# Kernel tuning notes

Hardware: AMD Instinct MI355X
Metric: run time of the kernel (lower is better)

Reference implementation:

```python
import jax, jax.numpy as jnp
import numpy as np

B, S, D, H = 2, 2048, 1024, 16
DK = D // H


def setup_inputs() -> dict:
    key = jax.random.key(0)
    ks = jax.random.split(key, 12)
    sd = 1.0 / np.sqrt(D)
    inp = {
        "query": jax.random.normal(ks[0], (B, S, D), jnp.float32),
        "key": jax.random.normal(ks[1], (B, S, D), jnp.float32),
        "value": jax.random.normal(ks[2], (B, S, D), jnp.float32),
        # causal mask, broadcast over batch and heads: [1, 1, S, S]
        "mask": jnp.tril(jnp.ones((S, S), jnp.bool_))[None, None],
        "wq_w": jax.random.uniform(ks[3], (D, D), jnp.float32, -sd, sd),
        "wq_b": jax.random.uniform(ks[4], (D,), jnp.float32, -sd, sd),
        "wk_w": jax.random.uniform(ks[5], (D, D), jnp.float32, -sd, sd),
        "wk_b": jax.random.uniform(ks[6], (D,), jnp.float32, -sd, sd),
        "wv_w": jax.random.uniform(ks[7], (D, D), jnp.float32, -sd, sd),
        "wv_b": jax.random.uniform(ks[8], (D,), jnp.float32, -sd, sd),
        "wo_w": jax.random.uniform(ks[9], (D, D), jnp.float32, -sd, sd),
        "wo_b": jax.random.uniform(ks[10], (D,), jnp.float32, -sd, sd),
    }
    return inp


def reference(query, key, value, mask, wq_w, wq_b, wk_w, wk_b, wv_w, wv_b, wo_w, wo_b):
    # linear projections (torch Linear: x @ W^T + b), split into heads -> [B, H, S, DK]
    def proj(x, w, b):
        y = jnp.einsum("bsd,ed->bse", x, w) + b
        return y.reshape(B, S, H, DK).transpose(0, 2, 1, 3)

    q = proj(query, wq_w, wq_b)
    k = proj(key, wk_w, wk_b)
    v = proj(value, wv_w, wv_b)

    scale = 1.0 / np.sqrt(DK)
    scores = jnp.einsum("bhqd,bhkd->bhqk", q, k) * scale  # [B, H, S, S]
    scores = jnp.where(mask, scores, -jnp.inf)
    attn = jax.nn.softmax(scores, axis=-1)
    out = jnp.einsum("bhqk,bhkd->bhqd", attn, v)  # [B, H, S, DK]
    out = out.transpose(0, 2, 1, 3).reshape(B, S, D)
    # output projection; dropout is identity at eval / p=0
    return jnp.einsum("bsd,ed->bse", out, wo_w) + wo_b
```

## Files before the change

kernel.cpp:

```cpp
#include <hip/hip_runtime.h>


typedef unsigned short u16;
typedef unsigned int u32;
typedef __bf16 bf16x8 __attribute__((ext_vector_type(8)));
typedef float f32x4 __attribute__((ext_vector_type(4)));
typedef float f32x16 __attribute__((ext_vector_type(16)));
typedef float f32x2 __attribute__((ext_vector_type(2)));
typedef float f32x4v __attribute__((ext_vector_type(4)));
typedef u16 u16x4 __attribute__((ext_vector_type(4)));
typedef u32 u32x4 __attribute__((ext_vector_type(4)));
typedef int i32x4 __attribute__((ext_vector_type(4)));

#define B_ 2
#define S_ 2048
#define D_ 1024
#define H_ 16
#define DK_ 64

__device__ __forceinline__ u16 f2bf(float f) {
  __bf16 h = (__bf16)f;
  return __builtin_bit_cast(u16, h);
}

__device__ __forceinline__ float fexp2(float x) { return __builtin_amdgcn_exp2f(x); }

__device__ __forceinline__ f32x4 mfma16(bf16x8 a, bf16x8 b, f32x4 c) {
  return __builtin_amdgcn_mfma_f32_16x16x32_bf16(a, b, c, 0, 0, 0);
}
__device__ __forceinline__ f32x16 mfma32(bf16x8 a, bf16x8 b, f32x16 c) {
  return __builtin_amdgcn_mfma_f32_32x32x16_bf16(a, b, c, 0, 0, 0);
}

__device__ __forceinline__ u32 cvtpk(float lo, float hi) {
  u32 r;
  asm volatile("v_cvt_pk_bf16_f32 %0, %1, %2" : "=v"(r) : "v"(lo), "v"(hi));
  return r;
}
__device__ __forceinline__ u32 sx32(u32 v) { return (u32)__shfl_xor((int)v, 32, 64); }

typedef __attribute__((address_space(1))) void GV;
typedef __attribute__((address_space(3))) void LV;
__device__ __forceinline__ void gload16(const u16* g, u16* l) {
  __builtin_amdgcn_global_load_lds((GV*)g, (LV*)l, 16, 0, 0);
}

__global__ __launch_bounds__(256) void cast_all(const float* __restrict__ s0, const float* __restrict__ s1,
                                                const float* __restrict__ s2, const float* __restrict__ s3,
                                                const float* __restrict__ s4, const float* __restrict__ s5,
                                                const float* __restrict__ s6, u16* __restrict__ dst) {
  const int N0 = 1048576, N1 = 2097152, N2 = 3145728, N3 = 3407872, N4 = 3670016, N5 = 3932160, N6 = 4194304;
  int stride = gridDim.x * blockDim.x;
  for (int i = blockIdx.x * blockDim.x + threadIdx.x; i < N6; i += stride) {
    const float* src;
    int off;
    if (i < N0)      { src = s0; off = i; }
    else if (i < N1) { src = s1; off = i - N0; }
    else if (i < N2) { src = s2; off = i - N1; }
    else if (i < N3) { src = s3; off = i - N2; }
    else if (i < N4) { src = s4; off = i - N3; }
    else if (i < N5) { src = s5; off = i - N4; }
    else             { src = s6; off = i - N5; }
    f32x4v v = reinterpret_cast<const f32x4v*>(src)[off];
    u16x4 o;
    o.x = f2bf(v.x); o.y = f2bf(v.y); o.z = f2bf(v.z); o.w = f2bf(v.w);
    reinterpret_cast<u16x4*>(dst)[i] = o;
  }
}

__device__ __forceinline__ void gemm_tile_128(const u16* __restrict__ A,
                                              const u16* __restrict__ Bw,
                                              int K, int bm, int bn,
                                              f32x4 (&acc)[4][4],
                                              u16* ldsA, u16* ldsB) {
  const int tid = threadIdx.x;
  const int lane = tid & 63;
  const int w = tid >> 6;
  const int wm = w >> 1, wn = w & 1;
  const int fr = lane & 15, fq = lane >> 4;

  const u16* aBase = A + (size_t)(bm * 128) * K;
  const u16* bBase = Bw + (size_t)(bn * 128) * K;

  const int r0 = tid >> 2;
  const int cq0 = tid & 3;
  const int cs0 = (cq0 ^ (r0 & 3)) * 8;
  const int cs1 = (cq0 ^ ((r0 + 64) & 3)) * 8;

#define STAGE_G(buf, kk)                                                                          \
  do {                                                                                            \
    gload16(aBase + (size_t)r0 * K + (kk) + cs0, ldsA + (buf) * 4096 + tid * 8);                  \
    gload16(aBase + (size_t)(r0 + 64) * K + (kk) + cs1, ldsA + (buf) * 4096 + (tid + 256) * 8);   \
    gload16(bBase + (size_t)r0 * K + (kk) + cs0, ldsB + (buf) * 4096 + tid * 8);                  \
    gload16(bBase + (size_t)(r0 + 64) * K + (kk) + cs1, ldsB + (buf) * 4096 + (tid + 256) * 8);   \
  } while (0)

  STAGE_G(0, 0);
  STAGE_G(1, 32);

  const int nk = K >> 5;
  for (int t = 0; t < nk; ++t) {
    if (t + 1 < nk) { asm volatile("s_waitcnt vmcnt(4)" ::: "memory"); }
    else            { asm volatile("s_waitcnt vmcnt(0)" ::: "memory"); }
    __builtin_amdgcn_s_barrier();
    __builtin_amdgcn_sched_barrier(0);
    if (t + 2 < nk) {
      const int nb = (t + 2) % 3;
      STAGE_G(nb, (t + 2) * 32);
    }
    const u16* la = ldsA + (t % 3) * 4096;
    const u16* lb = ldsB + (t % 3) * 4096;
    bf16x8 af[4], bfv[4];
#pragma unroll
    for (int m = 0; m < 4; ++m) {
      int row = wm * 64 + m * 16 + fr;
      int cq = fq ^ (row & 3);
      af[m] = *reinterpret_cast<const bf16x8*>(la + (row * 4 + cq) * 8);
    }
#pragma unroll
    for (int n = 0; n < 4; ++n) {
      int row = wn * 64 + n * 16 + fr;
      int cq = fq ^ (row & 3);
      bfv[n] = *reinterpret_cast<const bf16x8*>(lb + (row * 4 + cq) * 8);
    }
    __builtin_amdgcn_s_setprio(1);
#pragma unroll
    for (int m = 0; m < 4; ++m)
#pragma unroll
      for (int n = 0; n < 4; ++n)
        acc[m][n] = mfma16(af[m], bfv[n], acc[m][n]);
    __builtin_amdgcn_s_setprio(0);
  }
#undef STAGE_G
}

__global__ __launch_bounds__(256) void gemm_qkv(const u16* __restrict__ Xq, const u16* __restrict__ Xk,
                                                const u16* __restrict__ Xv, const u16* __restrict__ Wq,
                                                const u16* __restrict__ Wk, const u16* __restrict__ Wv,
                                                const float* __restrict__ bq, const float* __restrict__ bk,
                                                const float* __restrict__ bv,
                                                u16* __restrict__ Qw, u16* __restrict__ Kw,
                                                u16* __restrict__ Vt) {
  __shared__ __align__(16) u16 ldsA[3 * 128 * 32];
  __shared__ __align__(16) u16 ldsB[3 * 128 * 32];
  const int z = blockIdx.z;
  const u16* A = (z == 0) ? Xq : (z == 1) ? Xk : Xv;
  const u16* W = (z == 0) ? Wq : (z == 1) ? Wk : Wv;
  const float* bias = (z == 0) ? bq : (z == 1) ? bk : bv;
  const float osc = (z == 0) ? (0.125f * 1.44269504f) : 1.0f;

  f32x4 acc[4][4];
#pragma unroll
  for (int m = 0; m < 4; ++m)
#pragma unroll
    for (int n = 0; n < 4; ++n)
      acc[m][n] = (f32x4){0.f, 0.f, 0.f, 0.f};

  gemm_tile_128(A, W, 1024, blockIdx.y, blockIdx.x, acc, ldsA, ldsB);

  const int lane = threadIdx.x & 63;
  const int w = threadIdx.x >> 6, wm = w >> 1, wn = w & 1;
  const int fr = lane & 15, fq = lane >> 4;
#pragma unroll
  for (int m = 0; m < 4; ++m) {
#pragma unroll
    for (int n = 0; n < 4; ++n) {
      int col = blockIdx.x * 128 + wn * 64 + n * 16 + fr;
      float bcol = bias[col];
      int h = col >> 6, dk = col & 63;
#pragma unroll
      for (int j = 0; j < 4; ++j) {
        int row = blockIdx.y * 128 + wm * 64 + m * 16 + fq * 4 + j;
        float v = (acc[m][n][j] + bcol) * osc;
        u16 bb = f2bf(v);
        int b = row >> 11, s = row & (S_ - 1);
        if (z == 0)      Qw[((b * H_ + h) * S_ + s) * DK_ + dk] = bb;
        else if (z == 1) Kw[((b * H_ + h) * S_ + s) * DK_ + dk] = bb;
        else             Vt[((b * H_ + h) * DK_ + dk) * S_ + s] = bb;
      }
    }
  }
}

__global__ __launch_bounds__(256) void gemm_out(const u16* __restrict__ O, const u16* __restrict__ Wo,
                                                const float* __restrict__ bo, float* __restrict__ Y) {
  __shared__ __align__(16) u16 ldsA[3 * 128 * 32];
  __shared__ __align__(16) u16 ldsB[3 * 128 * 32];
  f32x4 acc[4][4];
#pragma unroll
  for (int m = 0; m < 4; ++m)
#pragma unroll
    for (int n = 0; n < 4; ++n)
      acc[m][n] = (f32x4){0.f, 0.f, 0.f, 0.f};

  gemm_tile_128(O, Wo, 1024, blockIdx.y, blockIdx.x, acc, ldsA, ldsB);

  const int lane = threadIdx.x & 63;
  const int w = threadIdx.x >> 6, wm = w >> 1, wn = w & 1;
  const int fr = lane & 15, fq = lane >> 4;
#pragma unroll
  for (int m = 0; m < 4; ++m) {
#pragma unroll
    for (int n = 0; n < 4; ++n) {
      int col = blockIdx.x * 128 + wn * 64 + n * 16 + fr;
      float bcol = bo[col];
#pragma unroll
      for (int j = 0; j < 4; ++j) {
        int row = blockIdx.y * 128 + wm * 64 + m * 16 + fq * 4 + j;
        Y[(size_t)row * D_ + col] = acc[m][n][j] + bcol;
      }
    }
  }
}

__global__ __launch_bounds__(256) void attn_kernel(const u16* __restrict__ Qw,
                                                   const u16* __restrict__ Kw,
                                                   const u16* __restrict__ Vt,
                                                   u16* __restrict__ O) {
  __shared__ float mbuf[2][64][64];
  __shared__ float mlbuf[2][64];

  const int id = blockIdx.x;
  const int bh = (id & 7) * 4 + ((id >> 3) & 3);
  const int qb = 31 - (id >> 5);
  const int tid = threadIdx.x;
  const int w = tid >> 6;
  const int lane = tid & 63;
  const int col = lane & 31;
  const int hi = lane >> 5;

  const u16* Qg = Qw + ((size_t)bh * S_ + qb * 64) * DK_;
  const u16* Kg = Kw + (size_t)bh * S_ * DK_;
  const u16* Vg = Vt + (size_t)bh * DK_ * S_;
  const int b = bh >> 4, h = bh & 15;

  bf16x8 qf[2][4];
#pragma unroll
  for (int qt = 0; qt < 2; ++qt)
#pragma unroll
    for (int c = 0; c < 4; ++c)
      qf[qt][c] = *reinterpret_cast<const bf16x8*>(Qg + (qt * 32 + col) * DK_ + c * 16 + hi * 8);

  f32x16 o[2][2];
  float ll[2] = {0.f, 0.f};
#pragma unroll
  for (int qt = 0; qt < 2; ++qt)
#pragma unroll
    for (int dt = 0; dt < 2; ++dt)
#pragma unroll
      for (int r = 0; r < 16; ++r) o[qt][dt][r] = 0.f;

  for (int t = w; t <= qb; t += 4) {
    const u16* Kt = Kg + (size_t)t * 64 * DK_;
    const u16* Vtt = Vg + t * 64;
    bf16x8 pa[2][4];
#pragma unroll
    for (int kt = 0; kt < 2; ++kt) {
      bf16x8 ka[4];
#pragma unroll
      for (int c = 0; c < 4; ++c)
        ka[c] = *reinterpret_cast<const bf16x8*>(Kt + (kt * 32 + col) * DK_ + c * 16 + hi * 8);
      f32x16 s0, s1;
#pragma unroll
      for (int r = 0; r < 16; ++r) { s0[r] = 0.f; s1[r] = 0.f; }
      __builtin_amdgcn_s_setprio(1);
#pragma unroll
      for (int c = 0; c < 4; ++c) {
        s0 = mfma32(ka[c], qf[0][c], s0);
        s1 = mfma32(ka[c], qf[1][c], s1);
      }
      __builtin_amdgcn_s_setprio(0);

      if (t == qb) {
#pragma unroll
        for (int r = 0; r < 16; ++r) {
          int krow = kt * 32 + (r & 3) + 8 * (r >> 2) + 4 * hi;
          if (krow > col) s0[r] = -1.0e30f;
          if (krow > 32 + col) s1[r] = -1.0e30f;
        }
      }
      float a0 = 0.f, a1 = 0.f;
#pragma unroll
      for (int r = 0; r < 16; ++r) {
        s0[r] = fexp2(s0[r]); a0 += s0[r];
        s1[r] = fexp2(s1[r]); a1 += s1[r];
      }
      ll[0] += a0; ll[1] += a1;

#pragma unroll
      for (int qt = 0; qt < 2; ++qt) {
        const f32x16& sv = qt ? s1 : s0;
        u32 g0 = cvtpk(sv[0], sv[1]),   g1 = cvtpk(sv[2], sv[3]);
        u32 g2 = cvtpk(sv[4], sv[5]),   g3 = cvtpk(sv[6], sv[7]);
        u32 g4 = cvtpk(sv[8], sv[9]),   g5 = cvtpk(sv[10], sv[11]);
        u32 g6 = cvtpk(sv[12], sv[13]), g7 = cvtpk(sv[14], sv[15]);
        u32 t0 = sx32(g0), t1 = sx32(g1), t2 = sx32(g2), t3 = sx32(g3);
        u32 t4 = sx32(g4), t5 = sx32(g5), t6 = sx32(g6), t7 = sx32(g7);
        u32x4 lo4, hi4;
        lo4.x = hi ? t2 : g0;  lo4.y = hi ? t3 : g1;
        lo4.z = hi ? g2 : t0;  lo4.w = hi ? g3 : t1;
        hi4.x = hi ? t6 : g4;  hi4.y = hi ? t7 : g5;
        hi4.z = hi ? g6 : t4;  hi4.w = hi ? g7 : t5;
        pa[qt][kt * 2 + 0] = __builtin_bit_cast(bf16x8, lo4);
        pa[qt][kt * 2 + 1] = __builtin_bit_cast(bf16x8, hi4);
      }
    }

    __builtin_amdgcn_s_setprio(1);
#pragma unroll
    for (int dt = 0; dt < 2; ++dt) {
#pragma unroll
      for (int kc = 0; kc < 4; ++kc) {
        bf16x8 vb = *reinterpret_cast<const bf16x8*>(Vtt + (size_t)(dt * 32 + col) * S_ + kc * 16 + hi * 8);
        o[0][dt] = mfma32(pa[0][kc], vb, o[0][dt]);
        o[1][dt] = mfma32(pa[1][kc], vb, o[1][dt]);
      }
    }
    __builtin_amdgcn_s_setprio(0);
  }

  ll[0] += __shfl_xor(ll[0], 32, 64);
  ll[1] += __shfl_xor(ll[1], 32, 64);

#define WRITE_PART(i)                                                         \
  do {                                                                        \
    _Pragma("unroll") for (int qt = 0; qt < 2; ++qt) {                        \
      _Pragma("unroll") for (int dt = 0; dt < 2; ++dt)                        \
        _Pragma("unroll") for (int r = 0; r < 16; ++r) {                      \
          int qrow = qt * 32 + (r & 3) + 8 * (r >> 2) + 4 * hi;               \
          mbuf[i][qrow][dt * 32 + col] = o[qt][dt][r];                        \
        }                                                                     \
      if (hi == 0) mlbuf[i][qt * 32 + col] = ll[qt];                          \
    }                                                                         \
  } while (0)
#define ADD_PART(i)                                                           \
  do {                                                                        \
    _Pragma("unroll") for (int qt = 0; qt < 2; ++qt) {                        \
      _Pragma("unroll") for (int dt = 0; dt < 2; ++dt)                        \
        _Pragma("unroll") for (int r = 0; r < 16; ++r) {                      \
          int qrow = qt * 32 + (r & 3) + 8 * (r >> 2) + 4 * hi;               \
          o[qt][dt][r] += mbuf[i][qrow][dt * 32 + col];                       \
        }                                                                     \
      ll[qt] += mlbuf[i][qt * 32 + col];                                      \
    }                                                                         \
  } while (0)

  if (w == 1) WRITE_PART(0);
  if (w == 3) WRITE_PART(1);
  __syncthreads();
  if (w == 0) ADD_PART(0);
  if (w == 2) ADD_PART(1);
  __syncthreads();
  if (w == 2) WRITE_PART(0);
  __syncthreads();
  if (w == 0) { ADD_PART(0); WRITE_PART(0); }
  __syncthreads();
#undef WRITE_PART
#undef ADD_PART

#pragma unroll
  for (int it = 0; it < 8; ++it) {
    int q = w * 16 + it * 2 + hi;
    f32x2 v = *reinterpret_cast<const f32x2*>(&mbuf[0][q][col * 2]);
    float linv = 1.f / mlbuf[0][q];
    u32 pk = cvtpk(v.x * linv, v.y * linv);
    *reinterpret_cast<u32*>(O + ((size_t)b * S_ + qb * 64 + q) * D_ + h * 64 + col * 2) = pk;
  }
}

extern "C" void kernel_launch(void* const* d_in, const int* in_sizes, int n_in,
                              void* d_out, int out_size, void* d_ws, size_t ws_size,
                              hipStream_t stream) {
  const float* q_in = (const float*)d_in[0];
  const float* k_in = (const float*)d_in[1];
  const float* v_in = (const float*)d_in[2];
  const float* wq = (const float*)d_in[4];
  const float* bq = (const float*)d_in[5];
  const float* wk = (const float*)d_in[6];
  const float* bk = (const float*)d_in[7];
  const float* wv = (const float*)d_in[8];
  const float* bv = (const float*)d_in[9];
  const float* wo = (const float*)d_in[10];
  const float* bo = (const float*)d_in[11];

  char* ws = (char*)d_ws;
  const size_t MB = 1024 * 1024;
  u16* Xq = (u16*)(ws + 0 * MB);
  u16* Xk = (u16*)(ws + 8 * MB);
  u16* Xv = (u16*)(ws + 16 * MB);
  u16* Wq = (u16*)(ws + 24 * MB);
  u16* Wk = (u16*)(ws + 26 * MB);
  u16* Wv = (u16*)(ws + 28 * MB);
  u16* Wo = (u16*)(ws + 30 * MB);
  u16* Qw = (u16*)(ws + 32 * MB);
  u16* Kw = (u16*)(ws + 40 * MB);
  u16* Vt = (u16*)(ws + 48 * MB);
  u16* Ob = (u16*)(ws + 0 * MB);

  cast_all<<<2048, 256, 0, stream>>>(q_in, k_in, v_in, wq, wk, wv, wo, (u16*)ws);
  gemm_qkv<<<dim3(8, 32, 3), 256, 0, stream>>>(Xq, Xk, Xv, Wq, Wk, Wv, bq, bk, bv, Qw, Kw, Vt);
  attn_kernel<<<1024, 256, 0, stream>>>(Qw, Kw, Vt, Ob);
  gemm_out<<<dim3(8, 32), 256, 0, stream>>>(Ob, Wo, bo, (float*)d_out);
}
```

Before: 132.8 us.

## Restructure attention to share LDS-staged K/V tiles across eight query-row waves

The attention kernel now uses 256 blocks of 512 threads. Each block covers a 256-row query chunk with one wave per 32 query rows. K and V tiles are loaded once per block into triple-buffered, XOR-swizzled LDS using async global-to-LDS loads, replacing per-wave direct global loads and the cross-wave LDS reduction of partial outputs. This cuts redundant K/V global traffic and the reduction epilogue. The cost is block-wide barriers per tile, idle waves past their diagonal, fewer blocks with uneven causal work, and scalar bf16 output stores.

```diff
diff --git a/kernel.cpp b/kernel.cpp
--- a/kernel.cpp
+++ b/kernel.cpp
@@ -6,11 +6,9 @@
 typedef __bf16 bf16x8 __attribute__((ext_vector_type(8)));
 typedef float f32x4 __attribute__((ext_vector_type(4)));
 typedef float f32x16 __attribute__((ext_vector_type(16)));
-typedef float f32x2 __attribute__((ext_vector_type(2)));
 typedef float f32x4v __attribute__((ext_vector_type(4)));
 typedef u16 u16x4 __attribute__((ext_vector_type(4)));
 typedef u32 u32x4 __attribute__((ext_vector_type(4)));
-typedef int i32x4 __attribute__((ext_vector_type(4)));
 
 #define B_ 2
 #define S_ 2048
@@ -22,7 +20,6 @@
   __bf16 h = (__bf16)f;
   return __builtin_bit_cast(u16, h);
 }
-
 __device__ __forceinline__ float fexp2(float x) { return __builtin_amdgcn_exp2f(x); }
 
 __device__ __forceinline__ f32x4 mfma16(bf16x8 a, bf16x8 b, f32x4 c) {
@@ -31,7 +28,6 @@
 __device__ __forceinline__ f32x16 mfma32(bf16x8 a, bf16x8 b, f32x16 c) {
   return __builtin_amdgcn_mfma_f32_32x32x16_bf16(a, b, c, 0, 0, 0);
 }
-
 __device__ __forceinline__ u32 cvtpk(float lo, float hi) {
   u32 r;
   asm volatile("v_cvt_pk_bf16_f32 %0, %1, %2" : "=v"(r) : "v"(lo), "v"(hi));
@@ -213,159 +209,141 @@
   }
 }
 
-__global__ __launch_bounds__(256) void attn_kernel(const u16* __restrict__ Qw,
+__global__ __launch_bounds__(512) void attn_kernel(const u16* __restrict__ Qw,
                                                    const u16* __restrict__ Kw,
                                                    const u16* __restrict__ Vt,
-                                                   u16* __restrict__ O) {
-  __shared__ float mbuf[2][64][64];
-  __shared__ float mlbuf[2][64];
+                                                   u16* __restrict__ Ob) {
+  __shared__ __align__(16) u16 Kl[3][64 * 64];
+  __shared__ __align__(16) u16 Vl[3][64 * 64];
+  __shared__ float lls[8][32];
 
   const int id = blockIdx.x;
   const int bh = (id & 7) * 4 + ((id >> 3) & 3);
-  const int qb = 31 - (id >> 5);
+  const int chunk = id >> 5;
   const int tid = threadIdx.x;
   const int w = tid >> 6;
   const int lane = tid & 63;
   const int col = lane & 31;
   const int hi = lane >> 5;
 
-  const u16* Qg = Qw + ((size_t)bh * S_ + qb * 64) * DK_;
   const u16* Kg = Kw + (size_t)bh * S_ * DK_;
   const u16* Vg = Vt + (size_t)bh * DK_ * S_;
   const int b = bh >> 4, h = bh & 15;
 
-  bf16x8 qf[2][4];
-#pragma unroll
-  for (int qt = 0; qt < 2; ++qt)
-#pragma unroll
-    for (int c = 0; c < 4; ++c)
-      qf[qt][c] = *reinterpret_cast<const bf16x8*>(Qg + (qt * 32 + col) * DK_ + c * 16 + hi * 8);
-
-  f32x16 o[2][2];
-  float ll[2] = {0.f, 0.f};
-#pragma unroll
-  for (int qt = 0; qt < 2; ++qt)
-#pragma unroll
-    for (int dt = 0; dt < 2; ++dt)
-#pragma unroll
-      for (int r = 0; r < 16; ++r) o[qt][dt][r] = 0.f;
-
-  for (int t = w; t <= qb; t += 4) {
-    const u16* Kt = Kg + (size_t)t * 64 * DK_;
-    const u16* Vtt = Vg + t * 64;
-    bf16x8 pa[2][4];
-#pragma unroll
-    for (int kt = 0; kt < 2; ++kt) {
-      bf16x8 ka[4];
-#pragma unroll
-      for (int c = 0; c < 4; ++c)
-        ka[c] = *reinterpret_cast<const bf16x8*>(Kt + (kt * 32 + col) * DK_ + c * 16 + hi * 8);
-      f32x16 s0, s1;
-#pragma unroll
-      for (int r = 0; r < 16; ++r) { s0[r] = 0.f; s1[r] = 0.f; }
+  const int qbase = chunk * 256 + w * 32;
+  const int tdiag = qbase >> 6;
+  const int nt = 4 * (chunk + 1);
+
+  const u16* Qg = Qw + ((size_t)bh * S_ + qbase) * DK_;
+  bf16x8 qf[4];
+#pragma unroll
+  for (int c = 0; c < 4; ++c)
+    qf[c] = *reinterpret_cast<const bf16x8*>(Qg + col * DK_ + c * 16 + hi * 8);
+
+  f32x16 o[2];
+  float ll = 0.f;
+#pragma unroll
+  for (int dt = 0; dt < 2; ++dt)
+#pragma unroll
+    for (int r = 0; r < 16; ++r) o[dt][r] = 0.f;
+
+  const int sr = tid >> 3;
+  const int scol = ((tid & 7) ^ (sr & 7)) * 8;
+
+#define STAGE_A(buf, t)                                                       \
+  do {                                                                        \
+    gload16(Kg + (size_t)((t) * 64 + sr) * DK_ + scol, &Kl[buf][tid * 8]);    \
+    gload16(Vg + (size_t)sr * S_ + (t) * 64 + scol, &Vl[buf][tid * 8]);       \
+  } while (0)
+
+  STAGE_A(0, 0);
+  STAGE_A(1, 1);
+
+  for (int t = 0; t < nt; ++t) {
+    if (t + 1 < nt) { asm volatile("s_waitcnt vmcnt(2)" ::: "memory"); }
+    else            { asm volatile("s_waitcnt vmcnt(0)" ::: "memory"); }
+    __builtin_amdgcn_s_barrier();
+    __builtin_amdgcn_sched_barrier(0);
+    if (t + 2 < nt) STAGE_A((t + 2) % 3, t + 2);
+
+    if (t <= tdiag) {
+      const u16* kl = Kl[t % 3];
+      const u16* vl = Vl[t % 3];
+      bf16x8 pa[4];
+#pragma unroll
+      for (int kt = 0; kt < 2; ++kt) {
+        bf16x8 ka[4];
+#pragma unroll
+        for (int c = 0; c < 4; ++c) {
+          int row = kt * 32 + col;
+          int e = (row * 64 + c * 16 + hi * 8) ^ ((row & 7) << 3);
+          ka[c] = *reinterpret_cast<const bf16x8*>(kl + e);
+        }
+        f32x16 s;
+#pragma unroll
+        for (int r = 0; r < 16; ++r) s[r] = 0.f;
+        __builtin_amdgcn_s_setprio(1);
+#pragma unroll
+        for (int c = 0; c < 4; ++c) s = mfma32(ka[c], qf[c], s);
+        __builtin_amdgcn_s_setprio(0);
+
+        if (t == tdiag) {
+#pragma unroll
+          for (int r = 0; r < 16; ++r) {
+            int krow = t * 64 + kt * 32 + (r & 3) + 8 * (r >> 2) + 4 * hi;
+            if (krow > qbase + col) s[r] = -1.0e30f;
+          }
+        }
+#pragma unroll
+        for (int r = 0; r < 16; ++r) { s[r] = fexp2(s[r]); ll += s[r]; }
+
+        {
+          u32 g0 = cvtpk(s[0], s[1]),   g1 = cvtpk(s[2], s[3]);
+          u32 g2 = cvtpk(s[4], s[5]),   g3 = cvtpk(s[6], s[7]);
+          u32 g4 = cvtpk(s[8], s[9]),   g5 = cvtpk(s[10], s[11]);
+          u32 g6 = cvtpk(s[12], s[13]), g7 = cvtpk(s[14], s[15]);
+          u32 x0 = sx32(g0), x1 = sx32(g1), x2 = sx32(g2), x3 = sx32(g3);
+          u32 x4 = sx32(g4), x5 = sx32(g5), x6 = sx32(g6), x7 = sx32(g7);
+          u32x4 lo4, hi4;
+          lo4.x = hi ? x2 : g0;  lo4.y = hi ? x3 : g1;
+          lo4.z = hi ? g2 : x0;  lo4.w = hi ? g3 : x1;
+          hi4.x = hi ? x6 : g4;  hi4.y = hi ? x7 : g5;
+          hi4.z = hi ? g6 : x4;  hi4.w = hi ? g7 : x5;
+          pa[kt * 2 + 0] = __builtin_bit_cast(bf16x8, lo4);
+          pa[kt * 2 + 1] = __builtin_bit_cast(bf16x8, hi4);
+        }
+      }
+
       __builtin_amdgcn_s_setprio(1);
 #pragma unroll
-      for (int c = 0; c < 4; ++c) {
-        s0 = mfma32(ka[c], qf[0][c], s0);
-        s1 = mfma32(ka[c], qf[1][c], s1);
+      for (int dt = 0; dt < 2; ++dt) {
+#pragma unroll
+        for (int kc = 0; kc < 4; ++kc) {
+          int row = dt * 32 + col;
+          int e = (row * 64 + kc * 16 + hi * 8) ^ ((row & 7) << 3);
+          bf16x8 vb = *reinterpret_cast<const bf16x8*>(vl + e);
+          o[dt] = mfma32(pa[kc], vb, o[dt]);
+        }
       }
       __builtin_amdgcn_s_setprio(0);
-
-      if (t == qb) {
-#pragma unroll
-        for (int r = 0; r < 16; ++r) {
-          int krow = kt * 32 + (r & 3) + 8 * (r >> 2) + 4 * hi;
-          if (krow > col) s0[r] = -1.0e30f;
-          if (krow > 32 + col) s1[r] = -1.0e30f;
-        }
-      }
-      float a0 = 0.f, a1 = 0.f;
-#pragma unroll
-      for (int r = 0; r < 16; ++r) {
-        s0[r] = fexp2(s0[r]); a0 += s0[r];
-        s1[r] = fexp2(s1[r]); a1 += s1[r];
-      }
-      ll[0] += a0; ll[1] += a1;
-
-#pragma unroll
-      for (int qt = 0; qt < 2; ++qt) {
-        const f32x16& sv = qt ? s1 : s0;
-        u32 g0 = cvtpk(sv[0], sv[1]),   g1 = cvtpk(sv[2], sv[3]);
-        u32 g2 = cvtpk(sv[4], sv[5]),   g3 = cvtpk(sv[6], sv[7]);
-        u32 g4 = cvtpk(sv[8], sv[9]),   g5 = cvtpk(sv[10], sv[11]);
-        u32 g6 = cvtpk(sv[12], sv[13]), g7 = cvtpk(sv[14], sv[15]);
-        u32 t0 = sx32(g0), t1 = sx32(g1), t2 = sx32(g2), t3 = sx32(g3);
-        u32 t4 = sx32(g4), t5 = sx32(g5), t6 = sx32(g6), t7 = sx32(g7);
-        u32x4 lo4, hi4;
-        lo4.x = hi ? t2 : g0;  lo4.y = hi ? t3 : g1;
-        lo4.z = hi ? g2 : t0;  lo4.w = hi ? g3 : t1;
-        hi4.x = hi ? t6 : g4;  hi4.y = hi ? t7 : g5;
-        hi4.z = hi ? g6 : t4;  hi4.w = hi ? g7 : t5;
-        pa[qt][kt * 2 + 0] = __builtin_bit_cast(bf16x8, lo4);
-        pa[qt][kt * 2 + 1] = __builtin_bit_cast(bf16x8, hi4);
-      }
-    }
-
-    __builtin_amdgcn_s_setprio(1);
-#pragma unroll
-    for (int dt = 0; dt < 2; ++dt) {
-#pragma unroll
-      for (int kc = 0; kc < 4; ++kc) {
-        bf16x8 vb = *reinterpret_cast<const bf16x8*>(Vtt + (size_t)(dt * 32 + col) * S_ + kc * 16 + hi * 8);
-        o[0][dt] = mfma32(pa[0][kc], vb, o[0][dt]);
-        o[1][dt] = mfma32(pa[1][kc], vb, o[1][dt]);
-      }
-    }
-    __builtin_amdgcn_s_setprio(0);
-  }
-
-  ll[0] += __shfl_xor(ll[0], 32, 64);
-  ll[1] += __shfl_xor(ll[1], 32, 64);
-
-#define WRITE_PART(i)                                                         \
-  do {                                                                        \
-    _Pragma("unroll") for (int qt = 0; qt < 2; ++qt) {                        \
-      _Pragma("unroll") for (int dt = 0; dt < 2; ++dt)                        \
-        _Pragma("unroll") for (int r = 0; r < 16; ++r) {                      \
-          int qrow = qt * 32 + (r & 3) + 8 * (r >> 2) + 4 * hi;               \
-          mbuf[i][qrow][dt * 32 + col] = o[qt][dt][r];                        \
-        }                                                                     \
-      if (hi == 0) mlbuf[i][qt * 32 + col] = ll[qt];                          \
-    }                                                                         \
-  } while (0)
-#define ADD_PART(i)                                                           \
-  do {                                                                        \
-    _Pragma("unroll") for (int qt = 0; qt < 2; ++qt) {                        \
-      _Pragma("unroll") for (int dt = 0; dt < 2; ++dt)                        \
-        _Pragma("unroll") for (int r = 0; r < 16; ++r) {                      \
-          int qrow = qt * 32 + (r & 3) + 8 * (r >> 2) + 4 * hi;               \
-          o[qt][dt][r] += mbuf[i][qrow][dt * 32 + col];                       \
-        }                                                                     \
-      ll[qt] += mlbuf[i][qt * 32 + col];                                      \
-    }                                                                         \
-  } while (0)
-
-  if (w == 1) WRITE_PART(0);
-  if (w == 3) WRITE_PART(1);
-  __syncthreads();
-  if (w == 0) ADD_PART(0);
-  if (w == 2) ADD_PART(1);
-  __syncthreads();
-  if (w == 2) WRITE_PART(0);
-  __syncthreads();
-  if (w == 0) { ADD_PART(0); WRITE_PART(0); }
-  __syncthreads();
-#undef WRITE_PART
-#undef ADD_PART
-
-#pragma unroll
-  for (int it = 0; it < 8; ++it) {
-    int q = w * 16 + it * 2 + hi;
-    f32x2 v = *reinterpret_cast<const f32x2*>(&mbuf[0][q][col * 2]);
-    float linv = 1.f / mlbuf[0][q];
-    u32 pk = cvtpk(v.x * linv, v.y * linv);
-    *reinterpret_cast<u32*>(O + ((size_t)b * S_ + qb * 64 + q) * D_ + h * 64 + col * 2) = pk;
-  }
+    }
+  }
+#undef STAGE_A
+
+  ll += __shfl_xor(ll, 32, 64);
+  if (hi == 0) lls[w][col] = ll;
+  float linv[16];
+#pragma unroll
+  for (int r = 0; r < 16; ++r)
+    linv[r] = 1.f / lls[w][(r & 3) + 8 * (r >> 2) + 4 * hi];
+
+#pragma unroll
+  for (int dt = 0; dt < 2; ++dt)
+#pragma unroll
+    for (int r = 0; r < 16; ++r) {
+      int q = qbase + (r & 3) + 8 * (r >> 2) + 4 * hi;
+      Ob[((size_t)b * S_ + q) * D_ + h * 64 + dt * 32 + col] = f2bf(o[dt][r] * linv[r]);
+    }
 }
 
 extern "C" void kernel_launch(void* const* d_in, const int* in_sizes, int n_in,
@@ -399,6 +377,6 @@
 
   cast_all<<<2048, 256, 0, stream>>>(q_in, k_in, v_in, wq, wk, wv, wo, (u16*)ws);
   gemm_qkv<<<dim3(8, 32, 3), 256, 0, stream>>>(Xq, Xk, Xv, Wq, Wk, Wv, bq, bk, bv, Qw, Kw, Vt);
-  attn_kernel<<<1024, 256, 0, stream>>>(Qw, Kw, Vt, Ob);
+  attn_kernel<<<256, 512, 0, stream>>>(Qw, Kw, Vt, Ob);
   gemm_out<<<dim3(8, 32), 256, 0, stream>>>(Ob, Wo, bo, (float*)d_out);
 }
```

Result: slower. 139.0 us (+4.7%).
